# Optimization experiments

Measured on AMD Instinct MI355X. Metric: run time of the kernel, lower is better.

Reference implementation:

```python
import jax, jax.numpy as jnp
import numpy as np
from jax import lax

N_BLOCKS = 5
POOL = 15
N_HEADS = 8
LATENT = 32
N_EXPERTS = 4


def setup_inputs() -> dict:
    key = jax.random.key(0)
    ks = jax.random.split(key, 24)
    B, T, D = 4, 2048, 512
    H = 2 * D  # expert_dim
    s = 0.02
    f = lambda k, shp: (jax.random.normal(k, shp, jnp.float32) * s)
    return {
        'x': jax.random.normal(ks[0], (B, T, D), jnp.float32),
        # TemporalGating gate_proj
        'tg_w': f(ks[1], (D, N_BLOCKS)), 'tg_b': jnp.zeros((N_BLOCKS,), jnp.float32),
        # DualScaleFusion
        'mp_w': f(ks[2], (D, D)), 'mp_b': jnp.zeros((D,), jnp.float32),
        'fu_w': f(ks[3], (2 * D, D)), 'fu_b': jnp.zeros((D,), jnp.float32),
        # MLAAttention (all no-bias)
        'wc': f(ks[4], (D, LATENT)), 'wk': f(ks[5], (LATENT, D)),
        'wv': f(ks[6], (LATENT, D)), 'wq': f(ks[7], (D, D)), 'wo': f(ks[8], (D, D)),
        # RMSNorms
        's1': jnp.ones((D,), jnp.float32), 's2': jnp.ones((D,), jnp.float32),
        # GatedMoE
        'wr': f(ks[9], (D, N_EXPERTS)), 'br': jnp.zeros((N_EXPERTS,), jnp.float32),
        'wg': f(ks[10], (D, D)), 'bg': jnp.zeros((D,), jnp.float32),
        'w1': f(ks[11], (N_EXPERTS, D, H)), 'b1': jnp.zeros((N_EXPERTS, H), jnp.float32),
        'w2': f(ks[12], (N_EXPERTS, H, D)), 'b2': jnp.zeros((N_EXPERTS, D), jnp.float32),
    }


def _temporal_gate(x, tg_w, tg_b):
    B, T, D = x.shape
    bs = T // N_BLOCKS
    tl = N_BLOCKS * bs
    r = x[:, :tl].reshape(B, N_BLOCKS, bs, D)          # [B,nb,bs,D]
    bm = r.mean(axis=2)                                 # [B,nb,D]
    imp = jax.nn.softmax(bm @ tg_w + tg_b, axis=-1)     # [B,nb,nb]
    imp = imp.mean(axis=-1, keepdims=True)              # [B,nb,1]
    g = (r * imp[..., None]).reshape(B, tl, D)
    return jnp.pad(g, ((0, 0), (0, T - tl), (0, 0)))


def _dual_scale(x, mp_w, mp_b, fu_w, fu_b):
    # AveragePooling1D(pool=15, stride=1, SAME): TF excludes padding from the mean.
    B, T, D = x.shape
    sums = lax.reduce_window(x, 0.0, lax.add, (1, POOL, 1), (1, 1, 1), 'SAME')
    cnt = lax.reduce_window(jnp.ones((1, T, 1), x.dtype), 0.0, lax.add,
                            (1, POOL, 1), (1, 1, 1), 'SAME')
    macro = sums / cnt
    macro_feat = macro @ mp_w + mp_b
    return jnp.concatenate([x, macro_feat], axis=-1) @ fu_w + fu_b


def _mla_attn(x, wc, wk, wv, wq, wo):
    B, T, D = x.shape
    dh = D // N_HEADS
    split = lambda t: t.reshape(B, T, N_HEADS, dh).transpose(0, 2, 1, 3)
    latent = x @ wc                                      # [B,T,L]
    K, V, Q = split(latent @ wk), split(latent @ wv), split(x @ wq)
    scores = jnp.einsum('bhqd,bhkd->bhqk', Q, K) / jnp.sqrt(jnp.float32(dh))
    causal = jnp.tril(jnp.ones((T, T), jnp.float32))
    scores = scores + (1.0 - causal) * -1e9
    attn = jax.nn.softmax(scores, axis=-1)
    out = jnp.einsum('bhqk,bhkd->bhqd', attn, V).transpose(0, 2, 1, 3).reshape(B, T, D)
    return out @ wo


def _rmsnorm(x, scale, eps=1e-6):
    var = jnp.mean(jnp.square(x), axis=-1, keepdims=True)
    return scale * (x * lax.rsqrt(var + eps))


def _moe(x, wr, br, wg, bg, w1, b1, w2, b2):
    w = jax.nn.softmax(x @ wr + br, axis=-1)             # [B,T,E]
    xg = x * jax.nn.sigmoid(x @ wg + bg)
    h = jax.nn.gelu(jnp.einsum('btd,edh->bteh', xg, w1) + b1, approximate=False)
    eo = jnp.einsum('bteh,ehd->bted', h, w2) + b2        # [B,T,E,D]
    return jnp.einsum('bted,bte->btd', eo, w)


def reference(x, tg_w, tg_b, mp_w, mp_b, fu_w, fu_b, wc, wk, wv, wq, wo,
              s1, s2, wr, br, wg, bg, w1, b1, w2, b2):
    xf = _temporal_gate(x, tg_w, tg_b)
    xfu = _dual_scale(xf, mp_w, mp_b, fu_w, fu_b)
    x1 = _rmsnorm(x + _mla_attn(xfu, wc, wk, wv, wq, wo), s1)
    return _rmsnorm(x1 + _moe(x1, wr, br, wg, bg, w1, b1, w2, b2), s2)
```

## Files before the change

### kernel.cpp

```cpp
#include <hip/hip_runtime.h>
#include <math.h>

#define B_   4
#define T_   2048
#define D_   512
#define TOK  (B_*T_)
#define TL_  2045
#define GATE 0.2f

typedef unsigned short u16;
typedef __attribute__((ext_vector_type(8))) short short8;
typedef __attribute__((ext_vector_type(4))) float f32x4;

static __device__ __forceinline__ u16 f2u(float f){
    union { float f; unsigned u; } a; a.f = f;
    unsigned r = a.u + 0x7fffu + ((a.u >> 16) & 1u);
    return (u16)(r >> 16);
}
static __device__ __forceinline__ float u2f(u16 u){
    union { unsigned u; float f; } a; a.u = ((unsigned)u) << 16;
    return a.f;
}
static __device__ __forceinline__ f32x4 mfma16(short8 a, short8 b, f32x4 c){
    return __builtin_amdgcn_mfma_f32_16x16x32_bf16(a, b, c, 0, 0, 0);
}
static __device__ __forceinline__ void glds16(const u16* g, u16* l){
    __builtin_amdgcn_global_load_lds((const __attribute__((address_space(1))) void*)g,
                                     (__attribute__((address_space(3))) void*)l, 16, 0, 0);
}

__global__ __launch_bounds__(256) void gatepool_kernel(
    const float* __restrict__ x, u16* __restrict__ xfcat)
{
    int idx = blockIdx.x*256 + threadIdx.x;
    int d = idx & 511, g = idx >> 9;
    int b = g >> 7, t0 = (g & 127) << 4;
    const float* xp = x + ((size_t)b*2048)*512 + d;
    float v[30];
    #pragma unroll
    for (int j = 0; j < 30; ++j){
        int u = t0 - 7 + j;
        v[j] = (u >= 0 && u < TL_) ? xp[(size_t)u*512] : 0.f;
    }
    float p[31]; p[0] = 0.f;
    #pragma unroll
    for (int j = 0; j < 30; ++j) p[j+1] = p[j] + v[j];
    u16* xc = xfcat + ((size_t)(b*2048 + t0))*1024 + d;
    #pragma unroll
    for (int i = 0; i < 16; ++i){
        int t = t0 + i;
        float sum = p[i+15] - p[i];
        int lo = t-7; if (lo < 0) lo = 0;
        int hi = t+7; if (hi > 2047) hi = 2047;
        xc[(size_t)i*1024]       = f2u((t < TL_) ? GATE*v[i+7] : 0.f);
        xc[(size_t)i*1024 + 512] = f2u(GATE * sum / (float)(hi - lo + 1));
    }
}

struct TJob { const float* src; u16* dst; int K, N, ldout, coloff, tiles; };
struct TJobs { TJob j[12]; int n; };

__global__ __launch_bounds__(256) void tconv_all_kernel(TJobs JJ){
    __shared__ float t[32][33];
    int idx = blockIdx.x;
    int jb = 0;
    while (jb < JJ.n - 1 && idx >= JJ.j[jb].tiles){ idx -= JJ.j[jb].tiles; ++jb; }
    TJob J = JJ.j[jb];
    int tX = J.N >> 5;
    int k0 = (idx / tX) * 32, n0 = (idx % tX) * 32;
    int tx = threadIdx.x & 31, ty = threadIdx.x >> 5;
    #pragma unroll
    for (int i = 0; i < 32; i += 8)
        t[ty+i][tx] = J.src[(size_t)(k0+ty+i)*J.N + n0+tx];
    __syncthreads();
    #pragma unroll
    for (int i = 0; i < 32; i += 8)
        J.dst[(size_t)(n0+ty+i)*J.ldout + J.coloff + k0+tx] = f2u(t[tx][ty+i]);
}

__global__ void convert_kernel(const float* __restrict__ in, u16* __restrict__ out){
    int idx = blockIdx.x*256 + threadIdx.x;
    out[idx] = f2u(in[idx]);
}

__global__ __launch_bounds__(256) void biasfold_kernel(
    const float* __restrict__ fu_b, const float* __restrict__ mp_b,
    const float* __restrict__ fu_w, float* __restrict__ out)
{
    int n = blockIdx.x, tid = threadIdx.x;
    float s = mp_b[tid]*fu_w[(size_t)(512+tid)*512 + n]
            + mp_b[tid+256]*fu_w[(size_t)(768+tid)*512 + n];
    for (int off = 32; off; off >>= 1) s += __shfl_down(s, off);
    __shared__ float ws[4];
    if ((tid & 63) == 0) ws[tid >> 6] = s;
    __syncthreads();
    if (tid == 0) out[n] = fu_b[n] + ws[0]+ws[1]+ws[2]+ws[3];
}

__global__ __launch_bounds__(256) void sgemm_kernel(const float* __restrict__ A,
    const float* __restrict__ B, u16* __restrict__ dstT, int ldT, int K){
    __shared__ float As[16][65];
    __shared__ float Bs[16][65];
    int tid = threadIdx.x;
    int tx = tid & 15, ty = tid >> 4;
    int m0 = blockIdx.y*64, n0 = blockIdx.x*64;
    int arow = tid >> 2, akq = (tid & 3) * 4;
    int bk = tid >> 4, bn = (tid & 15) * 4;
    float acc[4][4] = {};
    for (int k0 = 0; k0 < K; k0 += 16){
        const float* Ap = A + (size_t)(m0+arow)*K + k0 + akq;
        As[akq+0][arow]=Ap[0]; As[akq+1][arow]=Ap[1];
        As[akq+2][arow]=Ap[2]; As[akq+3][arow]=Ap[3];
        const float* Bp = B + (size_t)(k0+bk)*512 + n0 + bn;
        Bs[bk][bn+0]=Bp[0]; Bs[bk][bn+1]=Bp[1];
        Bs[bk][bn+2]=Bp[2]; Bs[bk][bn+3]=Bp[3];
        __syncthreads();
        #pragma unroll
        for (int kk = 0; kk < 16; ++kk){
            float av[4], bv[4];
            #pragma unroll
            for (int i=0;i<4;++i) av[i]=As[kk][ty*4+i];
            #pragma unroll
            for (int j=0;j<4;++j) bv[j]=Bs[kk][tx*4+j];
            #pragma unroll
            for (int i=0;i<4;++i)
                #pragma unroll
                for (int j=0;j<4;++j) acc[i][j] += av[i]*bv[j];
        }
        __syncthreads();
    }
    #pragma unroll
    for (int i=0;i<4;++i)
        #pragma unroll
        for (int j=0;j<4;++j)
            dstT[(size_t)(n0+tx*4+j)*ldT + m0+ty*4+i] = f2u(acc[i][j]);
}

#define GF_GELU   1
#define GF_ACCUM  2
#define GF_RSCOL  4
#define GF_GLU    8
#define GF_F32OUT 16
#define GF_TRANS  32

__global__ __launch_bounds__(256) void mgemm_kernel(
    const u16* __restrict__ A, int lda, const u16* __restrict__ Bt, int ldb,
    const float* __restrict__ bias, const float* __restrict__ rs,
    const u16* __restrict__ glu, void* __restrict__ Cp, int ldc,
    int K, int flags)
{
    __shared__ u16 As[128*64];
    __shared__ u16 Bs[128*64];
    int tid = threadIdx.x;
    int wave = tid >> 6, lane = tid & 63;
    int n16 = lane & 15, quad = lane >> 4;
    int m0 = blockIdx.y * 128, n0 = blockIdx.x * 128;
    int wr = (wave >> 1) * 64, wc = (wave & 1) * 64;

    f32x4 acc[4][4] = {};

    for (int k0 = 0; k0 < K; k0 += 64){
        #pragma unroll
        for (int i = 0; i < 4; ++i){
            int s = i*256 + tid;
            int row = s >> 3, gp = s & 7;
            int g = gp ^ (row & 7);
            glds16(A  + (size_t)(m0+row)*lda + k0 + g*8, As + (size_t)s*8);
            glds16(Bt + (size_t)(n0+row)*ldb + k0 + g*8, Bs + (size_t)s*8);
        }
        __syncthreads();
        #pragma unroll
        for (int ks = 0; ks < 2; ++ks){
            short8 af[4], bf[4];
            #pragma unroll
            for (int mi = 0; mi < 4; ++mi){
                int row = wr + mi*16 + n16;
                int g = (ks*4 + quad) ^ (row & 7);
                af[mi] = *(const short8*)&As[row*64 + g*8];
            }
            #pragma unroll
            for (int ni = 0; ni < 4; ++ni){
                int row = wc + ni*16 + n16;
                int g = (ks*4 + quad) ^ (row & 7);
                bf[ni] = *(const short8*)&Bs[row*64 + g*8];
            }
            #pragma unroll
            for (int mi = 0; mi < 4; ++mi)
                #pragma unroll
                for (int ni = 0; ni < 4; ++ni)
                    acc[mi][ni] = mfma16(af[mi], bf[ni], acc[mi][ni]);
        }
        __syncthreads();
    }

    if (flags & GF_TRANS){
        #pragma unroll
        for (int mi = 0; mi < 4; ++mi){
            int row0 = m0 + wr + mi*16 + quad*4;
            #pragma unroll
            for (int ni = 0; ni < 4; ++ni){
                int col = n0 + wc + ni*16 + n16;
                ushort4 h4;
                h4.x = f2u(acc[mi][ni][0]); h4.y = f2u(acc[mi][ni][1]);
                h4.z = f2u(acc[mi][ni][2]); h4.w = f2u(acc[mi][ni][3]);
                *(ushort4*)&((u16*)Cp)[(size_t)col*ldc + row0] = h4;
            }
        }
        return;
    }

    #pragma unroll
    for (int mi = 0; mi < 4; ++mi){
        #pragma unroll
        for (int reg = 0; reg < 4; ++reg){
            int row = m0 + wr + mi*16 + quad*4 + reg;
            #pragma unroll
            for (int ni = 0; ni < 4; ++ni){
                int col = n0 + wc + ni*16 + n16;
                float v = acc[mi][ni][reg];
                if (bias) v += bias[col];
                if (flags & GF_GELU)  v = 0.5f*v*(1.f + erff(v*0.70710678118f));
                if (flags & GF_GLU)   v = u2f(glu[(size_t)row*512 + col]) / (1.f + __expf(-v));
                if (flags & GF_RSCOL) v *= rs[(size_t)row*4 + (col >> 10)];
                size_t ci = (size_t)row*ldc + col;
                if (flags & GF_ACCUM)       ((float*)Cp)[ci] += v;
                else if (flags & GF_F32OUT) ((float*)Cp)[ci]  = v;
                else                        ((u16*)Cp)[ci]    = f2u(v);
            }
        }
    }
}

__global__ __launch_bounds__(256) void flash_kernel(
    const u16* __restrict__ QK,
    const u16* __restrict__ VT,
    u16* __restrict__ O)
{
    int bid = blockIdx.x;
    int qt = 15 - (bid & 15);
    int h = (bid >> 4) & 7, b = bid >> 7;
    __shared__ u16 Ks[64*64];
    __shared__ u16 Vt[64*64];
    __shared__ u16 Ps[4][32*64];
    int tid = threadIdx.x;
    int wave = tid >> 6, lane = tid & 63;
    int n16 = lane & 15, quad = lane >> 4;
    size_t btok = (size_t)b*2048;
    size_t tok0 = btok + qt*128;
    int rowbase[2];
    rowbase[0] = qt*128 + wave*32;
    rowbase[1] = rowbase[0] + 16;

    short8 aq[2][2];
    #pragma unroll
    for (int mi = 0; mi < 2; ++mi)
        #pragma unroll
        for (int ks = 0; ks < 2; ++ks)
            aq[mi][ks] = *(const short8*)&QK[(tok0 + wave*32 + mi*16 + n16)*1024
                                            + h*64 + ks*32 + quad*8];

    float m_st[2][4], l_st[2][4];
    #pragma unroll
    for (int mi = 0; mi < 2; ++mi)
        #pragma unroll
        for (int r = 0; r < 4; ++r){ m_st[mi][r] = -3.0e38f; l_st[mi][r] = 0.f; }
    f32x4 ov[2][4] = {};

    int nkt = 2*qt + 2;
    for (int kt = 0; kt < nkt; ++kt){
        __syncthreads();
        {
            int r = tid >> 2;
            int g0 = (tid & 3) * 2;
            const uint4* kp = (const uint4*)&QK[(btok + kt*64 + r)*1024 + 512 + h*64 + g0*8];
            uint4 ka = kp[0], kb = kp[1];
            *(uint4*)&Ks[r*64 + ((g0  ) ^ (r&7))*8] = ka;
            *(uint4*)&Ks[r*64 + ((g0+1) ^ (r&7))*8] = kb;
            const uint4* vp = (const uint4*)&VT[(size_t)(h*64 + r)*8192 + btok + kt*64 + g0*8];
            uint4 va = vp[0], vb = vp[1];
            *(uint4*)&Vt[r*64 + ((g0  ) ^ (r&7))*8] = va;
            *(uint4*)&Vt[r*64 + ((g0+1) ^ (r&7))*8] = vb;
        }
        __syncthreads();

        #pragma unroll
        for (int mi = 0; mi < 2; ++mi){
            if (kt*64 > rowbase[mi] + 15) continue;
            f32x4 s[4];
            #pragma unroll
            for (int ct = 0; ct < 4; ++ct){
                f32x4 a = {};
                #pragma unroll
                for (int ks = 0; ks < 2; ++ks){
                    short8 bk = *(const short8*)&Ks[(ct*16+n16)*64 + (((ks*4+quad) ^ (n16&7))*8)];
                    a = mfma16(aq[mi][ks], bk, a);
                }
                s[ct] = a * 0.125f;
            }
            if (kt*64 + 63 > rowbase[mi]){
                #pragma unroll
                for (int ct = 0; ct < 4; ++ct){
                    int col = kt*64 + ct*16 + n16;
                    #pragma unroll
                    for (int r = 0; r < 4; ++r)
                        if (col > rowbase[mi] + quad*4 + r) s[ct][r] = -3.0e38f;
                }
            }
            #pragma unroll
            for (int r = 0; r < 4; ++r){
                float mx = fmaxf(fmaxf(s[0][r], s[1][r]), fmaxf(s[2][r], s[3][r]));
                #pragma unroll
                for (int off = 1; off < 16; off <<= 1) mx = fmaxf(mx, __shfl_xor(mx, off));
                float mn = fmaxf(m_st[mi][r], mx);
                float al = __expf(m_st[mi][r] - mn);
                m_st[mi][r] = mn;
                float sum = 0.f;
                #pragma unroll
                for (int ct = 0; ct < 4; ++ct){
                    float p = __expf(s[ct][r] - mn);
                    s[ct][r] = p; sum += p;
                }
                #pragma unroll
                for (int off = 1; off < 16; off <<= 1) sum += __shfl_xor(sum, off);
                l_st[mi][r] = l_st[mi][r]*al + sum;
                #pragma unroll
                for (int dt = 0; dt < 4; ++dt) ov[mi][dt][r] *= al;
            }
            #pragma unroll
            for (int ct = 0; ct < 4; ++ct){
                int gg = ct*2 + (n16 >> 3);
                #pragma unroll
                for (int r = 0; r < 4; ++r){
                    int row = mi*16 + quad*4 + r;
                    Ps[wave][row*64 + ((gg ^ (row&7))*8) + (n16 & 7)] = f2u(s[ct][r]);
                }
            }
        }
        #pragma unroll
        for (int mi = 0; mi < 2; ++mi){
            if (kt*64 > rowbase[mi] + 15) continue;
            short8 ap[2];
            #pragma unroll
            for (int ks = 0; ks < 2; ++ks){
                int row = mi*16 + n16;
                ap[ks] = *(const short8*)&Ps[wave][row*64 + (((ks*4+quad) ^ (n16&7))*8)];
            }
            #pragma unroll
            for (int dt = 0; dt < 4; ++dt)
                #pragma unroll
                for (int ks = 0; ks < 2; ++ks){
                    short8 bv = *(const short8*)&Vt[(dt*16+n16)*64 + (((ks*4+quad) ^ (n16&7))*8)];
                    ov[mi][dt] = mfma16(ap[ks], bv, ov[mi][dt]);
                }
        }
    }
    #pragma unroll
    for (int mi = 0; mi < 2; ++mi)
        #pragma unroll
        for (int r = 0; r < 4; ++r){
            float inv = 1.f / l_st[mi][r];
            size_t row = tok0 + wave*32 + mi*16 + quad*4 + r;
            #pragma unroll
            for (int dt = 0; dt < 4; ++dt)
                O[row*512 + h*64 + dt*16 + n16] = f2u(ov[mi][dt][r] * inv);
        }
}

__global__ __launch_bounds__(256) void rmsnorm_kernel(
    const float* __restrict__ x, const u16* __restrict__ y,
    const float* __restrict__ scale, u16* __restrict__ out)
{
    int tok = blockIdx.x, tid = threadIdx.x;
    size_t base = (size_t)tok * 512;
    float v0 = x[base+tid]     + u2f(y[base+tid]);
    float v1 = x[base+tid+256] + u2f(y[base+tid+256]);
    float ss = v0*v0 + v1*v1;
    for (int off = 32; off; off >>= 1) ss += __shfl_down(ss, off);
    __shared__ float ws[4];
    if ((tid & 63) == 0) ws[tid >> 6] = ss;
    __syncthreads();
    float rstd = rsqrtf((ws[0]+ws[1]+ws[2]+ws[3])*(1.f/512.f) + 1e-6f);
    out[base+tid]     = f2u(scale[tid]     * v0 * rstd);
    out[base+tid+256] = f2u(scale[tid+256] * v1 * rstd);
}

__global__ __launch_bounds__(256) void final_kernel(
    const u16* __restrict__ x1, const float* __restrict__ moe,
    const float* __restrict__ rout, const float* __restrict__ b2,
    const float* __restrict__ scale, float* __restrict__ out)
{
    int tok = blockIdx.x, tid = threadIdx.x;
    size_t base = (size_t)tok * 512;
    float r0 = rout[tok*4+0], r1 = rout[tok*4+1], r2 = rout[tok*4+2], r3 = rout[tok*4+3];
    float bb0 = r0*b2[tid]     + r1*b2[512+tid]     + r2*b2[1024+tid]     + r3*b2[1536+tid];
    float bb1 = r0*b2[tid+256] + r1*b2[768+tid]     + r2*b2[1280+tid]     + r3*b2[1792+tid];
    float v0 = u2f(x1[base+tid])     + moe[base+tid]     + bb0;
    float v1 = u2f(x1[base+tid+256]) + moe[base+tid+256] + bb1;
    float ss = v0*v0 + v1*v1;
    for (int off = 32; off; off >>= 1) ss += __shfl_down(ss, off);
    __shared__ float ws[4];
    if ((tid & 63) == 0) ws[tid >> 6] = ss;
    __syncthreads();
    float rstd = rsqrtf((ws[0]+ws[1]+ws[2]+ws[3])*(1.f/512.f) + 1e-6f);
    out[base+tid]     = scale[tid]     * v0 * rstd;
    out[base+tid+256] = scale[tid+256] * v1 * rstd;
}

__global__ __launch_bounds__(256) void router_kernel(
    const u16* __restrict__ x1, const float* __restrict__ wr,
    const float* __restrict__ br, float* __restrict__ rout)
{
    int wid = threadIdx.x >> 6, lane = threadIdx.x & 63;
    int tok = blockIdx.x*4 + wid;
    const u16* xp = x1 + (size_t)tok*512;
    float p0=0.f, p1=0.f, p2=0.f, p3=0.f;
    for (int d = lane; d < 512; d += 64){
        float xv = u2f(xp[d]);
        p0 += xv*wr[d*4+0]; p1 += xv*wr[d*4+1];
        p2 += xv*wr[d*4+2]; p3 += xv*wr[d*4+3];
    }
    for (int off = 32; off; off >>= 1){
        p0 += __shfl_down(p0,off); p1 += __shfl_down(p1,off);
        p2 += __shfl_down(p2,off); p3 += __shfl_down(p3,off);
    }
    if (lane == 0){
        p0 += br[0]; p1 += br[1]; p2 += br[2]; p3 += br[3];
        float mx = fmaxf(fmaxf(p0,p1), fmaxf(p2,p3));
        float e0=__expf(p0-mx), e1=__expf(p1-mx), e2=__expf(p2-mx), e3=__expf(p3-mx);
        float inv = 1.f/(e0+e1+e2+e3);
        rout[tok*4+0]=e0*inv; rout[tok*4+1]=e1*inv;
        rout[tok*4+2]=e2*inv; rout[tok*4+3]=e3*inv;
    }
}

extern "C" void kernel_launch(void* const* d_in, const int* in_sizes, int n_in,
                              void* d_out, int out_size, void* d_ws, size_t ws_size,
                              hipStream_t stream)
{
    const float* x    = (const float*)d_in[0];
    const float* mp_w = (const float*)d_in[3];
    const float* mp_b = (const float*)d_in[4];
    const float* fu_w = (const float*)d_in[5];
    const float* fu_b = (const float*)d_in[6];
    const float* wc   = (const float*)d_in[7];
    const float* wk   = (const float*)d_in[8];
    const float* wv   = (const float*)d_in[9];
    const float* wq   = (const float*)d_in[10];
    const float* wo   = (const float*)d_in[11];
    const float* s1   = (const float*)d_in[12];
    const float* s2   = (const float*)d_in[13];
    const float* wr   = (const float*)d_in[14];
    const float* br   = (const float*)d_in[15];
    const float* wg   = (const float*)d_in[16];
    const float* bg   = (const float*)d_in[17];
    const float* w1   = (const float*)d_in[18];
    const float* b1   = (const float*)d_in[19];
    const float* w2   = (const float*)d_in[20];
    const float* b2   = (const float*)d_in[21];

    char* wsb = (char*)d_ws;
    const size_t MB = 1024*1024;
    u16*   wqkT   = (u16*)(wsb + 0);
    u16*   wcvT   = (u16*)(wsb + 1*MB);
    u16*   woT    = (u16*)(wsb + (3*MB)/2);
    u16*   wgT    = (u16*)(wsb + 2*MB);
    u16*   WfuT2  = (u16*)(wsb + (5*MB)/2);
    u16*   fuBT   = (u16*)(wsb + (7*MB)/2);
    u16*   mp_wB  = (u16*)(wsb + 4*MB);
    u16*   w1T    = (u16*)(wsb + (9*MB)/2);
    u16*   w2Ts   = (u16*)(wsb + (17*MB)/2);
    float* fubias = (float*)(wsb + (25*MB)/2);
    float* ROUT   = (float*)(wsb + (25*MB)/2 + 4096);
    u16*   XFcat = (u16*)(wsb + 13*MB);
    float* MOE   = (float*)(wsb + 13*MB);
    u16*   S3    = (u16*)(wsb + 13*MB);
    u16*   XFU   = (u16*)(wsb + 29*MB);
    u16*   XG    = (u16*)(wsb + 29*MB);
    u16*   QKb   = (u16*)(wsb + 37*MB);
    u16*   Hb    = (u16*)(wsb + 37*MB);
    u16*   VbT   = (u16*)(wsb + 53*MB);
    u16*   ATT   = (u16*)(wsb + 61*MB);
    u16*   x1h   = (u16*)(wsb + 69*MB);

    auto mg = [&](const u16* A, int lda, const u16* Bt, int ldb, const float* bias,
                  const float* rs, const u16* glu, void* C, int ldc,
                  int M, int N, int K, int flags){
        dim3 g(N/128, M/128);
        mgemm_kernel<<<g, 256, 0, stream>>>(A, lda, Bt, ldb, bias, rs, glu, C, ldc, K, flags);
    };

    TJobs JJ; JJ.n = 11;
    auto setj = [&](int i, const float* src, u16* dst, int K, int N, int ldout, int coloff){
        JJ.j[i] = TJob{src, dst, K, N, ldout, coloff, (K/32)*(N/32)};
    };
    setj(0, wq,            wqkT,  512,  512,  512, 0);
    setj(1, wo,            woT,   512,  512,  512, 0);
    setj(2, wg,            wgT,   512,  512,  512, 0);
    setj(3, fu_w,          WfuT2, 512,  512, 1024, 0);
    setj(4, fu_w + 512*512,fuBT,  512,  512,  512, 0);
    int nt = 5*256;
    for (int e = 0; e < 4; ++e){
        setj(5+e, w1 + (size_t)e*512*1024, w1T + (size_t)e*1024*512, 512, 1024, 512, 0);
        nt += 512;
    }
    JJ.n = 12;
    setj(9,  w2,                      w2Ts, 1024, 512, 4096, 0);
    setj(10, w2 + (size_t)1*1024*512, w2Ts, 1024, 512, 4096, 1024);
    setj(11, w2 + (size_t)2*1024*512, w2Ts, 1024, 512, 4096, 2048);
    nt += 3*512;
    tconv_all_kernel<<<nt, 256, 0, stream>>>(JJ);
    TJobs J2; J2.n = 1;
    J2.j[0] = TJob{w2 + (size_t)3*1024*512, w2Ts, 1024, 512, 4096, 3072, 512};
    tconv_all_kernel<<<512, 256, 0, stream>>>(J2);
    convert_kernel<<<512*512/256, 256, 0, stream>>>(mp_w, mp_wB);
    sgemm_kernel<<<dim3(8,8), 256, 0, stream>>>(wc, wk, wqkT + 512*512, 512, 32);
    sgemm_kernel<<<dim3(8,8), 256, 0, stream>>>(wc, wv, wcvT, 512, 32);
    biasfold_kernel<<<512, 256, 0, stream>>>(fu_b, mp_b, fu_w, fubias);
    mg(fuBT, 512, mp_wB, 512, 0, 0, 0, WfuT2 + 512, 1024, 512, 512, 512, 0);

    gatepool_kernel<<<(TOK/16)*512/256, 256, 0, stream>>>(x, XFcat);
    mg(XFcat, 1024, WfuT2, 1024, fubias, 0, 0, XFU, 512, TOK, 512, 1024, 0);
    mg(XFU, 512, wqkT, 512, 0, 0, 0, QKb, 1024, TOK, 1024, 512, 0);
    mg(XFU, 512, wcvT, 512, 0, 0, 0, VbT, 8192, TOK, 512, 512, GF_TRANS);
    flash_kernel<<<512, 256, 0, stream>>>(QKb, VbT, ATT);
    mg(ATT, 512, woT, 512, 0, 0, 0, S3, 512, TOK, 512, 512, 0);
    rmsnorm_kernel<<<TOK, 256, 0, stream>>>(x, S3, s1, x1h);
    router_kernel<<<TOK/4, 256, 0, stream>>>(x1h, wr, br, ROUT);
    mg(x1h, 512, wgT, 512, bg, 0, x1h, XG, 512, TOK, 512, 512, GF_GLU);
    for (int p = 0; p < 2; ++p){
        mg(XG, 512, w1T + (size_t)p*2048*512, 512, b1 + p*2048, ROUT + p*2, 0,
           Hb, 2048, TOK, 2048, 512, GF_GELU | GF_RSCOL);
        mg(Hb, 2048, w2Ts + p*2048, 4096, 0, 0, 0,
           MOE, 512, TOK, 512, 2048, p ? GF_ACCUM : GF_F32OUT);
    }
    final_kernel<<<TOK, 256, 0, stream>>>(x1h, MOE, ROUT, b2, s2, (float*)d_out);
}
```

Measured before the change: 697.0 us.

## Add 64-row GEMM tile variant, fold attention scale into Wq, reorder flash blocks

```diff
diff --git a/kernel.cpp b/kernel.cpp
--- a/kernel.cpp
+++ b/kernel.cpp
@@ -57,7 +57,7 @@
     }
 }
 
-struct TJob { const float* src; u16* dst; int K, N, ldout, coloff, tiles; };
+struct TJob { const float* src; u16* dst; int K, N, ldout, coloff, tiles; float scale; };
 struct TJobs { TJob j[12]; int n; };
 
 __global__ __launch_bounds__(256) void tconv_all_kernel(TJobs JJ){
@@ -75,7 +75,7 @@
     __syncthreads();
     #pragma unroll
     for (int i = 0; i < 32; i += 8)
-        J.dst[(size_t)(n0+ty+i)*J.ldout + J.coloff + k0+tx] = f2u(t[tx][ty+i]);
+        J.dst[(size_t)(n0+ty+i)*J.ldout + J.coloff + k0+tx] = f2u(J.scale * t[tx][ty+i]);
 }
 
 __global__ void convert_kernel(const float* __restrict__ in, u16* __restrict__ out){
@@ -143,37 +143,43 @@
 #define GF_F32OUT 16
 #define GF_TRANS  32
 
+template<int MT>
 __global__ __launch_bounds__(256) void mgemm_kernel(
     const u16* __restrict__ A, int lda, const u16* __restrict__ Bt, int ldb,
     const float* __restrict__ bias, const float* __restrict__ rs,
     const u16* __restrict__ glu, void* __restrict__ Cp, int ldc,
     int K, int flags)
 {
-    __shared__ u16 As[128*64];
+    constexpr int MI = MT/32;
+    __shared__ u16 As[MT*64];
     __shared__ u16 Bs[128*64];
     int tid = threadIdx.x;
     int wave = tid >> 6, lane = tid & 63;
     int n16 = lane & 15, quad = lane >> 4;
-    int m0 = blockIdx.y * 128, n0 = blockIdx.x * 128;
-    int wr = (wave >> 1) * 64, wc = (wave & 1) * 64;
-
-    f32x4 acc[4][4] = {};
+    int m0 = blockIdx.y * MT, n0 = blockIdx.x * 128;
+    int wr = (wave >> 1) * (MT/2), wc = (wave & 1) * 64;
+
+    f32x4 acc[MI][4] = {};
 
     for (int k0 = 0; k0 < K; k0 += 64){
+        #pragma unroll
+        for (int i = 0; i < MT/32; ++i){
+            int s = i*256 + tid;
+            int row = s >> 3, g = (s & 7) ^ (row & 7);
+            glds16(A + (size_t)(m0+row)*lda + k0 + g*8, As + (size_t)s*8);
+        }
         #pragma unroll
         for (int i = 0; i < 4; ++i){
             int s = i*256 + tid;
-            int row = s >> 3, gp = s & 7;
-            int g = gp ^ (row & 7);
-            glds16(A  + (size_t)(m0+row)*lda + k0 + g*8, As + (size_t)s*8);
+            int row = s >> 3, g = (s & 7) ^ (row & 7);
             glds16(Bt + (size_t)(n0+row)*ldb + k0 + g*8, Bs + (size_t)s*8);
         }
         __syncthreads();
         #pragma unroll
         for (int ks = 0; ks < 2; ++ks){
-            short8 af[4], bf[4];
-            #pragma unroll
-            for (int mi = 0; mi < 4; ++mi){
+            short8 af[MI], bf[4];
+            #pragma unroll
+            for (int mi = 0; mi < MI; ++mi){
                 int row = wr + mi*16 + n16;
                 int g = (ks*4 + quad) ^ (row & 7);
                 af[mi] = *(const short8*)&As[row*64 + g*8];
@@ -185,7 +191,7 @@
                 bf[ni] = *(const short8*)&Bs[row*64 + g*8];
             }
             #pragma unroll
-            for (int mi = 0; mi < 4; ++mi)
+            for (int mi = 0; mi < MI; ++mi)
                 #pragma unroll
                 for (int ni = 0; ni < 4; ++ni)
                     acc[mi][ni] = mfma16(af[mi], bf[ni], acc[mi][ni]);
@@ -195,7 +201,7 @@
 
     if (flags & GF_TRANS){
         #pragma unroll
-        for (int mi = 0; mi < 4; ++mi){
+        for (int mi = 0; mi < MI; ++mi){
             int row0 = m0 + wr + mi*16 + quad*4;
             #pragma unroll
             for (int ni = 0; ni < 4; ++ni){
@@ -210,7 +216,7 @@
     }
 
     #pragma unroll
-    for (int mi = 0; mi < 4; ++mi){
+    for (int mi = 0; mi < MI; ++mi){
         #pragma unroll
         for (int reg = 0; reg < 4; ++reg){
             int row = m0 + wr + mi*16 + quad*4 + reg;
@@ -237,8 +243,9 @@
     u16* __restrict__ O)
 {
     int bid = blockIdx.x;
-    int qt = 15 - (bid & 15);
-    int h = (bid >> 4) & 7, b = bid >> 7;
+    int qt = 15 - (bid >> 5);
+    int bh = bid & 31;
+    int h = bh & 7, b = bh >> 3;
     __shared__ u16 Ks[64*64];
     __shared__ u16 Vt[64*64];
     __shared__ u16 Ps[4][32*64];
@@ -295,7 +302,7 @@
                     short8 bk = *(const short8*)&Ks[(ct*16+n16)*64 + (((ks*4+quad) ^ (n16&7))*8)];
                     a = mfma16(aq[mi][ks], bk, a);
                 }
-                s[ct] = a * 0.125f;
+                s[ct] = a;
             }
             if (kt*64 + 63 > rowbase[mi]){
                 #pragma unroll
@@ -482,56 +489,63 @@
     u16*   ATT   = (u16*)(wsb + 61*MB);
     u16*   x1h   = (u16*)(wsb + 69*MB);
 
-    auto mg = [&](const u16* A, int lda, const u16* Bt, int ldb, const float* bias,
-                  const float* rs, const u16* glu, void* C, int ldc,
-                  int M, int N, int K, int flags){
+    auto mg128 = [&](const u16* A, int lda, const u16* Bt, int ldb, const float* bias,
+                     const float* rs, const u16* glu, void* C, int ldc,
+                     int M, int N, int K, int flags){
         dim3 g(N/128, M/128);
-        mgemm_kernel<<<g, 256, 0, stream>>>(A, lda, Bt, ldb, bias, rs, glu, C, ldc, K, flags);
+        mgemm_kernel<128><<<g, 256, 0, stream>>>(A, lda, Bt, ldb, bias, rs, glu, C, ldc, K, flags);
     };
-
-    TJobs JJ; JJ.n = 11;
-    auto setj = [&](int i, const float* src, u16* dst, int K, int N, int ldout, int coloff){
-        JJ.j[i] = TJob{src, dst, K, N, ldout, coloff, (K/32)*(N/32)};
+    auto mg64 = [&](const u16* A, int lda, const u16* Bt, int ldb, const float* bias,
+                    const float* rs, const u16* glu, void* C, int ldc,
+                    int M, int N, int K, int flags){
+        dim3 g(N/128, M/64);
+        mgemm_kernel<64><<<g, 256, 0, stream>>>(A, lda, Bt, ldb, bias, rs, glu, C, ldc, K, flags);
     };
-    setj(0, wq,            wqkT,  512,  512,  512, 0);
-    setj(1, wo,            woT,   512,  512,  512, 0);
-    setj(2, wg,            wgT,   512,  512,  512, 0);
-    setj(3, fu_w,          WfuT2, 512,  512, 1024, 0);
-    setj(4, fu_w + 512*512,fuBT,  512,  512,  512, 0);
+
+    TJobs JJ;
+    auto setj = [&](int i, const float* src, u16* dst, int K, int N, int ldout,
+                    int coloff, float scale){
+        JJ.j[i] = TJob{src, dst, K, N, ldout, coloff, (K/32)*(N/32), scale};
+    };
+    setj(0, wq,            wqkT,  512,  512,  512, 0, 0.125f);
+    setj(1, wo,            woT,   512,  512,  512, 0, 1.f);
+    setj(2, wg,            wgT,   512,  512,  512, 0, 1.f);
+    setj(3, fu_w,          WfuT2, 512,  512, 1024, 0, 1.f);
+    setj(4, fu_w + 512*512,fuBT,  512,  512,  512, 0, 1.f);
     int nt = 5*256;
     for (int e = 0; e < 4; ++e){
-        setj(5+e, w1 + (size_t)e*512*1024, w1T + (size_t)e*1024*512, 512, 1024, 512, 0);
+        setj(5+e, w1 + (size_t)e*512*1024, w1T + (size_t)e*1024*512, 512, 1024, 512, 0, 1.f);
         nt += 512;
     }
     JJ.n = 12;
-    setj(9,  w2,                      w2Ts, 1024, 512, 4096, 0);
-    setj(10, w2 + (size_t)1*1024*512, w2Ts, 1024, 512, 4096, 1024);
-    setj(11, w2 + (size_t)2*1024*512, w2Ts, 1024, 512, 4096, 2048);
+    setj(9,  w2,                      w2Ts, 1024, 512, 4096, 0,    1.f);
+    setj(10, w2 + (size_t)1*1024*512, w2Ts, 1024, 512, 4096, 1024, 1.f);
+    setj(11, w2 + (size_t)2*1024*512, w2Ts, 1024, 512, 4096, 2048, 1.f);
     nt += 3*512;
     tconv_all_kernel<<<nt, 256, 0, stream>>>(JJ);
     TJobs J2; J2.n = 1;
-    J2.j[0] = TJob{w2 + (size_t)3*1024*512, w2Ts, 1024, 512, 4096, 3072, 512};
+    J2.j[0] = TJob{w2 + (size_t)3*1024*512, w2Ts, 1024, 512, 4096, 3072, 512, 1.f};
     tconv_all_kernel<<<512, 256, 0, stream>>>(J2);
     convert_kernel<<<512*512/256, 256, 0, stream>>>(mp_w, mp_wB);
     sgemm_kernel<<<dim3(8,8), 256, 0, stream>>>(wc, wk, wqkT + 512*512, 512, 32);
     sgemm_kernel<<<dim3(8,8), 256, 0, stream>>>(wc, wv, wcvT, 512, 32);
     biasfold_kernel<<<512, 256, 0, stream>>>(fu_b, mp_b, fu_w, fubias);
-    mg(fuBT, 512, mp_wB, 512, 0, 0, 0, WfuT2 + 512, 1024, 512, 512, 512, 0);
+    mg64(fuBT, 512, mp_wB, 512, 0, 0, 0, WfuT2 + 512, 1024, 512, 512, 512, 0);
 
     gatepool_kernel<<<(TOK/16)*512/256, 256, 0, stream>>>(x, XFcat);
-    mg(XFcat, 1024, WfuT2, 1024, fubias, 0, 0, XFU, 512, TOK, 512, 1024, 0);
-    mg(XFU, 512, wqkT, 512, 0, 0, 0, QKb, 1024, TOK, 1024, 512, 0);
-    mg(XFU, 512, wcvT, 512, 0, 0, 0, VbT, 8192, TOK, 512, 512, GF_TRANS);
+    mg64 (XFcat, 1024, WfuT2, 1024, fubias, 0, 0, XFU, 512, TOK, 512, 1024, 0);
+    mg128(XFU, 512, wqkT, 512, 0, 0, 0, QKb, 1024, TOK, 1024, 512, 0);
+    mg64 (XFU, 512, wcvT, 512, 0, 0, 0, VbT, 8192, TOK, 512, 512, GF_TRANS);
     flash_kernel<<<512, 256, 0, stream>>>(QKb, VbT, ATT);
-    mg(ATT, 512, woT, 512, 0, 0, 0, S3, 512, TOK, 512, 512, 0);
+    mg64 (ATT, 512, woT, 512, 0, 0, 0, S3, 512, TOK, 512, 512, 0);
     rmsnorm_kernel<<<TOK, 256, 0, stream>>>(x, S3, s1, x1h);
     router_kernel<<<TOK/4, 256, 0, stream>>>(x1h, wr, br, ROUT);
-    mg(x1h, 512, wgT, 512, bg, 0, x1h, XG, 512, TOK, 512, 512, GF_GLU);
+    mg64 (x1h, 512, wgT, 512, bg, 0, x1h, XG, 512, TOK, 512, 512, GF_GLU);
     for (int p = 0; p < 2; ++p){
-        mg(XG, 512, w1T + (size_t)p*2048*512, 512, b1 + p*2048, ROUT + p*2, 0,
-           Hb, 2048, TOK, 2048, 512, GF_GELU | GF_RSCOL);
-        mg(Hb, 2048, w2Ts + p*2048, 4096, 0, 0, 0,
-           MOE, 512, TOK, 512, 2048, p ? GF_ACCUM : GF_F32OUT);
+        mg128(XG, 512, w1T + (size_t)p*2048*512, 512, b1 + p*2048, ROUT + p*2, 0,
+              Hb, 2048, TOK, 2048, 512, GF_GELU | GF_RSCOL);
+        mg64 (Hb, 2048, w2Ts + p*2048, 4096, 0, 0, 0,
+              MOE, 512, TOK, 512, 2048, p ? GF_ACCUM : GF_F32OUT);
     }
     final_kernel<<<TOK, 256, 0, stream>>>(x1h, MOE, ROUT, b2, s2, (float*)d_out);
 }
```

Result: faster. 631.3 us (-9.4%).
